# Kernel optimization log

Measured on AMD Instinct MI355X. Metric: run time of the kernel, lower is better.

The kernel has to match this reference:

```python
import jax, jax.numpy as jnp
import numpy as np

B, S, D, H = 4, 1024, 1024, 16
DH = D // H  # head dim = 64
NEG = 1e9  # keras Softmax masking constant for fp32


def setup_inputs() -> dict:
    key = jax.random.key(0)
    ks = jax.random.split(key, 7)
    return {
        "inputs": jax.random.normal(ks[0], (B, S, D), jnp.float32),
        "mask": jax.random.randint(ks[1], (B, 1, 1, S), 0, 2) > 0,
        "interaction": jax.random.normal(ks[2], (B, S, S, H), jnp.float32) * 0.1,
        "W_Q": jax.random.normal(ks[3], (D, D), jnp.float32) * 0.02,
        "W_K": jax.random.normal(ks[4], (D, D), jnp.float32) * 0.02,
        "W_V": jax.random.normal(ks[5], (D, D), jnp.float32) * 0.02,
        "W_O": jax.random.normal(ks[6], (D, D), jnp.float32) * 0.02,
    }


def reference(inputs, mask, interaction, W_Q, W_K, W_V, W_O):
    b, s, d = inputs.shape
    def proj(W):
        # [B,S,D] @ [D,D] -> [B,S,H,DH] -> [B,H,S,DH]
        return (inputs @ W).reshape(b, s, H, DH).transpose(0, 2, 1, 3)
    Q, K, V = proj(W_Q), proj(W_K), proj(W_V)
    scores = jnp.einsum("bhqd,bhkd->bhqk", Q, K) / (DH ** 0.5)
    # interaction [B,S,S,H] -> [B,H,S,S], additive bias before softmax
    scores = scores + interaction.transpose(0, 3, 1, 2)
    # keras Softmax(mask=...): add -1e9 where mask is False, softmax over last axis
    scores = jnp.where(mask, scores, scores - NEG)
    attn = jax.nn.softmax(scores, axis=-1)
    hidden = jnp.einsum("bhqk,bhkd->bhqd", attn, V)
    hidden = hidden.transpose(0, 2, 1, 3).reshape(b, s, d)
    return hidden @ W_O
```

## Files before the change

### kernel.cpp

```cpp
#include <hip/hip_runtime.h>
#include <hip/hip_bf16.h>
#include <stdint.h>

#define BDIM 4
#define SDIM 1024
#define DDIM 1024
#define HDIM 16
#define DHDIM 64

typedef __bf16 bf16_t;
typedef __bf16 bf16x8 __attribute__((ext_vector_type(8)));
typedef __bf16 bf16x4 __attribute__((ext_vector_type(4)));
typedef float f32x4 __attribute__((ext_vector_type(4)));

typedef __attribute__((address_space(3))) uint32_t lds_u32;
typedef const __attribute__((address_space(1))) uint32_t glb_u32;

__device__ __forceinline__ void glds16(const void* g, void* l) {
    __builtin_amdgcn_global_load_lds((glb_u32*)g, (lds_u32*)l, 16, 0, 0);
}


__global__ __launch_bounds__(256) void convert_x_kernel(const float* __restrict__ X,
                                                        bf16_t* __restrict__ Xb, int n) {
    int i = (blockIdx.x * 256 + threadIdx.x) * 4;
    if (i >= n) return;
    float4 v = *(const float4*)(X + i);
    bf16x4 o;
    o[0] = (bf16_t)v.x; o[1] = (bf16_t)v.y; o[2] = (bf16_t)v.z; o[3] = (bf16_t)v.w;
    *(bf16x4*)(Xb + i) = o;
}

__global__ __launch_bounds__(256) void transpose_w_kernel(const float* __restrict__ W0,
                                                          const float* __restrict__ W1,
                                                          const float* __restrict__ W2,
                                                          const float* __restrict__ W3,
                                                          bf16_t* __restrict__ Wt) {
    __shared__ float tile[32][33];
    int z = blockIdx.z;
    const float* W = (z == 0) ? W0 : (z == 1) ? W1 : (z == 2) ? W2 : W3;
    bf16_t* dst = Wt + (size_t)z * DDIM * DDIM;
    int bx = blockIdx.x * 32;
    int by = blockIdx.y * 32;
    int x = threadIdx.x & 31, y0 = threadIdx.x >> 5;
#pragma unroll
    for (int i = 0; i < 4; i++) {
        int y = y0 + i * 8;
        tile[y][x] = W[(size_t)(by + y) * DDIM + bx + x];
    }
    __syncthreads();
#pragma unroll
    for (int i = 0; i < 4; i++) {
        int y = y0 + i * 8;
        dst[(size_t)(bx + y) * DDIM + by + x] = (bf16_t)tile[x][y];
    }
}

__global__ __launch_bounds__(256) void mask_flag_kernel(const unsigned char* __restrict__ mb,
                                                        int* __restrict__ flag) {
    __shared__ int any;
    if (threadIdx.x == 0) any = 0;
    __syncthreads();
    int loc = 0;
    for (int i = threadIdx.x; i < BDIM * SDIM; i += 256)
        if ((i & 3) && mb[i]) loc = 1;
    if (loc) any = 1;
    __syncthreads();
    if (threadIdx.x == 0) *flag = any ? 1 : 0;
}

__global__ __launch_bounds__(256) void bias_tr_kernel(const float* __restrict__ inter,
                                                      const unsigned char* __restrict__ maskb,
                                                      const int* __restrict__ flagp,
                                                      bf16_t* __restrict__ biasT) {
    constexpr int QS = 72;
    constexpr int HS = 16 * 72 + 8;
    __shared__ bf16_t tile[16 * HS];
    __shared__ float pen[64];
    const int k0 = blockIdx.x * 64;
    const int q0 = blockIdx.y * 16;
    const int b  = blockIdx.z;
    const int t = threadIdx.x;
    const int mstride = (*flagp) ? 1 : 4;
    if (t < 64)
        pen[t] = maskb[((size_t)b * SDIM + k0 + t) * mstride] ? 0.f : 1.0e9f;

    const float* src = inter + (((size_t)b * SDIM + q0) * SDIM + k0) * HDIM;
    const int k = t >> 2, h = (t & 3) * 4;
#pragma unroll
    for (int q = 0; q < 16; q++) {
        float4 v = *(const float4*)(src + (size_t)q * SDIM * HDIM + t * 4);
        tile[(h + 0) * HS + q * QS + k] = (bf16_t)v.x;
        tile[(h + 1) * HS + q * QS + k] = (bf16_t)v.y;
        tile[(h + 2) * HS + q * QS + k] = (bf16_t)v.z;
        tile[(h + 3) * HS + q * QS + k] = (bf16_t)v.w;
    }
    __syncthreads();
#pragma unroll
    for (int p = 0; p < 8; p++) {
        int row = p * 32 + (t >> 3);
        int hh = row >> 4, qq = row & 15;
        int kc = (t & 7) * 8;
        bf16x8 vv = *(const bf16x8*)(tile + hh * HS + qq * QS + kc);
        bf16x8 ov;
#pragma unroll
        for (int u = 0; u < 8; u++) ov[u] = (bf16_t)((float)vv[u] - pen[kc + u]);
        *(bf16x8*)(biasT + ((size_t)(b * HDIM + hh) * SDIM + q0 + qq) * SDIM + k0 + kc) = ov;
    }
}

template <int MODE>
__global__ __launch_bounds__(256) void gemm_bt_kernel(const bf16_t* __restrict__ A,
                                                      const bf16_t* __restrict__ Bt,
                                                      bf16_t* __restrict__ Qo, bf16_t* __restrict__ Ko,
                                                      bf16_t* __restrict__ Vo, float* __restrict__ Co) {
    __shared__ bf16_t As[128 * 32];
    __shared__ bf16_t Bs[128 * 32];
    const int m0 = blockIdx.x * 128;
    const int n0 = blockIdx.y * 128;
    const int t = threadIdx.x;
    const int lane = t & 63, w = t >> 6;
    const int wm = w & 1, wn = w >> 1;
    const int low = lane & 15, quad = lane >> 4;
    f32x4 acc[4][4] = {};

    const int srow = w * 16 + (lane >> 2);
    const int koff = (lane & 3) * 8;
    const bf16_t* Ag = A + (size_t)(m0 + srow) * DDIM + koff;
    const bf16_t* Bg = Bt + (size_t)(n0 + srow) * DDIM + koff;
    bf16_t* AsW = As + w * 512;
    bf16_t* BsW = Bs + w * 512;

    for (int k0 = 0; k0 < DDIM; k0 += 32) {
        __syncthreads();
        glds16(Ag + k0, AsW);
        glds16(Ag + (size_t)64 * DDIM + k0, AsW + 64 * 32);
        glds16(Bg + k0, BsW);
        glds16(Bg + (size_t)64 * DDIM + k0, BsW + 64 * 32);
        __syncthreads();
        bf16x8 af[4], bv[4];
#pragma unroll
        for (int mt = 0; mt < 4; mt++)
            af[mt] = *(const bf16x8*)(As + (wm * 64 + mt * 16 + low) * 32 + quad * 8);
#pragma unroll
        for (int nt = 0; nt < 4; nt++)
            bv[nt] = *(const bf16x8*)(Bs + (wn * 64 + nt * 16 + low) * 32 + quad * 8);
#pragma unroll
        for (int mt = 0; mt < 4; mt++)
#pragma unroll
            for (int nt = 0; nt < 4; nt++)
                acc[mt][nt] = __builtin_amdgcn_mfma_f32_16x16x32_bf16(af[mt], bv[nt], acc[mt][nt], 0, 0, 0);
    }

#pragma unroll
    for (int mt = 0; mt < 4; mt++) {
#pragma unroll
        for (int nt = 0; nt < 4; nt++) {
#pragma unroll
            for (int r = 0; r < 4; r++) {
                int mrow = m0 + wm * 64 + mt * 16 + quad * 4 + r;
                int ncol = n0 + wn * 64 + nt * 16 + low;
                float vv = acc[mt][nt][r];
                if (MODE == 0) {
                    int which = ncol >> 10, nl = ncol & 1023;
                    int h = nl >> 6, dh = nl & 63;
                    int b = mrow >> 10, s = mrow & 1023;
                    size_t idx = ((size_t)(b * HDIM + h) * SDIM + s) * DHDIM + dh;
                    if (which == 0) Qo[idx] = (bf16_t)(vv * 0.125f);
                    else if (which == 1) Ko[idx] = (bf16_t)vv;
                    else Vo[idx] = (bf16_t)vv;
                } else {
                    Co[(size_t)mrow * DDIM + ncol] = vv;
                }
            }
        }
    }
}

__global__ __launch_bounds__(256) void attn_kernel(const bf16_t* __restrict__ Q,
                                                   const bf16_t* __restrict__ K,
                                                   const bf16_t* __restrict__ V,
                                                   const bf16_t* __restrict__ biasT,
                                                   bf16_t* __restrict__ hid) {
    __shared__ bf16_t Vt[64 * 72];
    __shared__ bf16_t P[4][16 * 72];
    const int bh = blockIdx.x;
    const int b = bh >> 4, h = bh & 15;
    const int q0 = blockIdx.y * 64;
    const int t = threadIdx.x;
    const int w = t >> 6, lane = t & 63;
    const int low = lane & 15, quad = lane >> 4;

    const bf16_t* Qb = Q + (size_t)bh * SDIM * DHDIM;
    const bf16_t* Kb = K + (size_t)bh * SDIM * DHDIM;
    const bf16_t* Vb = V + (size_t)bh * SDIM * DHDIM;
    const bf16_t* biasB = biasT + (size_t)bh * SDIM * SDIM;

    const int qrow = q0 + w * 16 + low;
    bf16x8 qf0 = *(const bf16x8*)(Qb + (size_t)qrow * DHDIM + quad * 8);
    bf16x8 qf1 = *(const bf16x8*)(Qb + (size_t)qrow * DHDIM + 32 + quad * 8);

    const int qr = q0 + w * 16 + quad * 4;

    float mrow[4], lrow[4];
    f32x4 accO[4] = {};
#pragma unroll
    for (int r = 0; r < 4; r++) { mrow[r] = -3.0e38f; lrow[r] = 0.f; }

    for (int kt = 0; kt < SDIM / 64; kt++) {
        const int kbase = kt * 64;
        __syncthreads();
        {
            int c0 = t, c1 = t + 256;
            int key0 = c0 >> 3, d0 = (c0 & 7) * 8;
            int key1 = c1 >> 3, d1 = (c1 & 7) * 8;
            bf16x8 v0 = *(const bf16x8*)(Vb + (size_t)(kbase + key0) * DHDIM + d0);
            bf16x8 v1 = *(const bf16x8*)(Vb + (size_t)(kbase + key1) * DHDIM + d1);
#pragma unroll
            for (int u = 0; u < 8; u++) Vt[(d0 + u) * 72 + key0] = v0[u];
#pragma unroll
            for (int u = 0; u < 8; u++) Vt[(d1 + u) * 72 + key1] = v1[u];
        }
        f32x4 sacc[4];
#pragma unroll
        for (int nt = 0; nt < 4; nt++) {
            int krow = kbase + nt * 16 + low;
            bf16x8 kf0 = *(const bf16x8*)(Kb + (size_t)krow * DHDIM + quad * 8);
            bf16x8 kf1 = *(const bf16x8*)(Kb + (size_t)krow * DHDIM + 32 + quad * 8);
            f32x4 z = {};
            z = __builtin_amdgcn_mfma_f32_16x16x32_bf16(qf0, kf0, z, 0, 0, 0);
            z = __builtin_amdgcn_mfma_f32_16x16x32_bf16(qf1, kf1, z, 0, 0, 0);
            sacc[nt] = z;
        }
        __syncthreads();
        float sv[4][4];
#pragma unroll
        for (int nt = 0; nt < 4; nt++) {
            int kk = kbase + nt * 16 + low;
#pragma unroll
            for (int r = 0; r < 4; r++) {
                float biasv = (float)biasB[(size_t)(qr + r) * SDIM + kk];
                sv[nt][r] = sacc[nt][r] + biasv;
            }
        }
#pragma unroll
        for (int r = 0; r < 4; r++) {
            float vmx = fmaxf(fmaxf(sv[0][r], sv[1][r]), fmaxf(sv[2][r], sv[3][r]));
            vmx = fmaxf(vmx, __shfl_xor(vmx, 1));
            vmx = fmaxf(vmx, __shfl_xor(vmx, 2));
            vmx = fmaxf(vmx, __shfl_xor(vmx, 4));
            vmx = fmaxf(vmx, __shfl_xor(vmx, 8));
            float mn = fmaxf(mrow[r], vmx);
            float alpha = __expf(mrow[r] - mn);
            mrow[r] = mn;
            lrow[r] *= alpha;
#pragma unroll
            for (int nt = 0; nt < 4; nt++) accO[nt][r] *= alpha;
            float rs = 0.f;
#pragma unroll
            for (int nt = 0; nt < 4; nt++) {
                float p = __expf(sv[nt][r] - mn);
                sv[nt][r] = p;
                rs += p;
            }
            rs += __shfl_xor(rs, 1);
            rs += __shfl_xor(rs, 2);
            rs += __shfl_xor(rs, 4);
            rs += __shfl_xor(rs, 8);
            lrow[r] += rs;
        }
        bf16_t* Pw = &P[w][0];
#pragma unroll
        for (int nt = 0; nt < 4; nt++)
#pragma unroll
            for (int r = 0; r < 4; r++)
                Pw[(quad * 4 + r) * 72 + nt * 16 + low] = (bf16_t)sv[nt][r];
        __syncthreads();
#pragma unroll
        for (int step = 0; step < 2; step++) {
            bf16x8 pf = *(const bf16x8*)(Pw + low * 72 + step * 32 + quad * 8);
#pragma unroll
            for (int nt = 0; nt < 4; nt++) {
                bf16x8 vf = *(const bf16x8*)(Vt + (nt * 16 + low) * 72 + step * 32 + quad * 8);
                accO[nt] = __builtin_amdgcn_mfma_f32_16x16x32_bf16(pf, vf, accO[nt], 0, 0, 0);
            }
        }
    }
#pragma unroll
    for (int r = 0; r < 4; r++) {
        float inv = 1.f / lrow[r];
#pragma unroll
        for (int nt = 0; nt < 4; nt++) {
            hid[((size_t)b * SDIM + (qr + r)) * DDIM + h * 64 + nt * 16 + low] =
                (bf16_t)(accO[nt][r] * inv);
        }
    }
}


extern "C" void kernel_launch(void* const* d_in, const int* in_sizes, int n_in,
                              void* d_out, int out_size, void* d_ws, size_t ws_size,
                              hipStream_t stream) {
    const float* X = (const float*)d_in[0];
    const unsigned char* maskb = (const unsigned char*)d_in[1];
    const float* inter = (const float*)d_in[2];
    const float* WQ = (const float*)d_in[3];
    const float* WK = (const float*)d_in[4];
    const float* WV = (const float*)d_in[5];
    const float* WO = (const float*)d_in[6];
    float* out = (float*)d_out;

    char* ws = (char*)d_ws;
    const size_t MB = 1024 * 1024;
    bf16_t* Xb    = (bf16_t*)(ws + 0 * MB);
    bf16_t* Wt    = (bf16_t*)(ws + 8 * MB);
    bf16_t* Qm    = (bf16_t*)(ws + 16 * MB);
    bf16_t* Km    = (bf16_t*)(ws + 24 * MB);
    bf16_t* Vm    = (bf16_t*)(ws + 32 * MB);
    bf16_t* hid   = (bf16_t*)(ws + 40 * MB);
    int* flag     = (int*)(ws + 48 * MB);
    bf16_t* biasT = (bf16_t*)(ws + 64 * MB);

    convert_x_kernel<<<BDIM * SDIM * DDIM / (256 * 4), 256, 0, stream>>>(X, Xb, BDIM * SDIM * DDIM);
    transpose_w_kernel<<<dim3(32, 32, 4), 256, 0, stream>>>(WQ, WK, WV, WO, Wt);
    mask_flag_kernel<<<1, 256, 0, stream>>>(maskb, flag);
    bias_tr_kernel<<<dim3(16, 64, 4), 256, 0, stream>>>(inter, maskb, flag, biasT);
    gemm_bt_kernel<0><<<dim3(32, 24), 256, 0, stream>>>(Xb, Wt, Qm, Km, Vm, nullptr);
    attn_kernel<<<dim3(BDIM * HDIM, SDIM / 64), 256, 0, stream>>>(Qm, Km, Vm, biasT, hid);
    gemm_bt_kernel<1><<<dim3(32, 8), 256, 0, stream>>>(hid, Wt + (size_t)3 * DDIM * DDIM,
                                                       nullptr, nullptr, nullptr, out);
}
```

Before: 570.0 us.

## Write V pre-transposed from QKV GEMM and drop block syncs in attention

The QKV projection epilogue now writes V in a [dh, s] transposed layout, so the attention kernel reads V^T fragments straight from global memory and no longer builds a transposed V tile in LDS. Each wave works independently with a per-wave fp32 LDS scratch that re-lays scores into row-per-lane form, which removes every __syncthreads and loads bias as contiguous bf16x8 vectors instead of scattered scalars. Softmax bookkeeping changes to one running max per lane with a cross-quad shuffle reduction, and occupancy is hinted via launch_bounds(256,4). The transposed V stores in the GEMM epilogue are strided, K and V are re-read from global by every wave without sharing, and the mask-flag kernel moves to 1024 threads.

```diff
diff --git a/kernel.cpp b/kernel.cpp
--- a/kernel.cpp
+++ b/kernel.cpp
@@ -56,13 +56,13 @@
     }
 }
 
-__global__ __launch_bounds__(256) void mask_flag_kernel(const unsigned char* __restrict__ mb,
-                                                        int* __restrict__ flag) {
+__global__ __launch_bounds__(1024) void mask_flag_kernel(const unsigned char* __restrict__ mb,
+                                                         int* __restrict__ flag) {
     __shared__ int any;
     if (threadIdx.x == 0) any = 0;
     __syncthreads();
     int loc = 0;
-    for (int i = threadIdx.x; i < BDIM * SDIM; i += 256)
+    for (int i = threadIdx.x; i < BDIM * SDIM; i += 1024)
         if ((i & 3) && mb[i]) loc = 1;
     if (loc) any = 1;
     __syncthreads();
@@ -113,7 +113,7 @@
 __global__ __launch_bounds__(256) void gemm_bt_kernel(const bf16_t* __restrict__ A,
                                                       const bf16_t* __restrict__ Bt,
                                                       bf16_t* __restrict__ Qo, bf16_t* __restrict__ Ko,
-                                                      bf16_t* __restrict__ Vo, float* __restrict__ Co) {
+                                                      bf16_t* __restrict__ Vto, float* __restrict__ Co) {
     __shared__ bf16_t As[128 * 32];
     __shared__ bf16_t Bs[128 * 32];
     const int m0 = blockIdx.x * 128;
@@ -165,10 +165,12 @@
                     int which = ncol >> 10, nl = ncol & 1023;
                     int h = nl >> 6, dh = nl & 63;
                     int b = mrow >> 10, s = mrow & 1023;
-                    size_t idx = ((size_t)(b * HDIM + h) * SDIM + s) * DHDIM + dh;
-                    if (which == 0) Qo[idx] = (bf16_t)(vv * 0.125f);
-                    else if (which == 1) Ko[idx] = (bf16_t)vv;
-                    else Vo[idx] = (bf16_t)vv;
+                    if (which == 0)
+                        Qo[((size_t)(b * HDIM + h) * SDIM + s) * DHDIM + dh] = (bf16_t)(vv * 0.125f);
+                    else if (which == 1)
+                        Ko[((size_t)(b * HDIM + h) * SDIM + s) * DHDIM + dh] = (bf16_t)vv;
+                    else
+                        Vto[((size_t)(b * HDIM + h) * DHDIM + dh) * SDIM + s] = (bf16_t)vv;
                 } else {
                     Co[(size_t)mrow * DDIM + ncol] = vv;
                 }
@@ -177,121 +179,113 @@
     }
 }
 
-__global__ __launch_bounds__(256) void attn_kernel(const bf16_t* __restrict__ Q,
-                                                   const bf16_t* __restrict__ K,
-                                                   const bf16_t* __restrict__ V,
-                                                   const bf16_t* __restrict__ biasT,
-                                                   bf16_t* __restrict__ hid) {
-    __shared__ bf16_t Vt[64 * 72];
-    __shared__ bf16_t P[4][16 * 72];
+__global__ __launch_bounds__(256, 4) void attn_kernel(const bf16_t* __restrict__ Q,
+                                                      const bf16_t* __restrict__ K,
+                                                      const bf16_t* __restrict__ Vt,
+                                                      const bf16_t* __restrict__ biasT,
+                                                      bf16_t* __restrict__ hid) {
+    constexpr int KSp = 66;
+    __shared__ float Sl[4][16 * KSp];
     const int bh = blockIdx.x;
     const int b = bh >> 4, h = bh & 15;
-    const int q0 = blockIdx.y * 64;
     const int t = threadIdx.x;
     const int w = t >> 6, lane = t & 63;
     const int low = lane & 15, quad = lane >> 4;
-
-    const bf16_t* Qb = Q + (size_t)bh * SDIM * DHDIM;
+    const int q0 = (blockIdx.y * 4 + w) * 16;
+
+    const bf16_t* Qb = Q + ((size_t)bh * SDIM + q0) * DHDIM;
     const bf16_t* Kb = K + (size_t)bh * SDIM * DHDIM;
-    const bf16_t* Vb = V + (size_t)bh * SDIM * DHDIM;
-    const bf16_t* biasB = biasT + (size_t)bh * SDIM * SDIM;
-
-    const int qrow = q0 + w * 16 + low;
-    bf16x8 qf0 = *(const bf16x8*)(Qb + (size_t)qrow * DHDIM + quad * 8);
-    bf16x8 qf1 = *(const bf16x8*)(Qb + (size_t)qrow * DHDIM + 32 + quad * 8);
-
-    const int qr = q0 + w * 16 + quad * 4;
-
-    float mrow[4], lrow[4];
+    const bf16_t* VtB = Vt + (size_t)bh * DHDIM * SDIM;
+    const bf16_t* biasB = biasT + ((size_t)bh * SDIM + q0 + low) * SDIM;
+    float* Sw = &Sl[w][0];
+
+    bf16x8 qf0 = *(const bf16x8*)(Qb + low * DHDIM + quad * 8);
+    bf16x8 qf1 = *(const bf16x8*)(Qb + low * DHDIM + 32 + quad * 8);
+
+    float mrow = -3.0e38f;
+    float lpart = 0.f;
     f32x4 accO[4] = {};
-#pragma unroll
-    for (int r = 0; r < 4; r++) { mrow[r] = -3.0e38f; lrow[r] = 0.f; }
-
-    for (int kt = 0; kt < SDIM / 64; kt++) {
-        const int kbase = kt * 64;
-        __syncthreads();
-        {
-            int c0 = t, c1 = t + 256;
-            int key0 = c0 >> 3, d0 = (c0 & 7) * 8;
-            int key1 = c1 >> 3, d1 = (c1 & 7) * 8;
-            bf16x8 v0 = *(const bf16x8*)(Vb + (size_t)(kbase + key0) * DHDIM + d0);
-            bf16x8 v1 = *(const bf16x8*)(Vb + (size_t)(kbase + key1) * DHDIM + d1);
-#pragma unroll
-            for (int u = 0; u < 8; u++) Vt[(d0 + u) * 72 + key0] = v0[u];
-#pragma unroll
-            for (int u = 0; u < 8; u++) Vt[(d1 + u) * 72 + key1] = v1[u];
-        }
+
+    for (int c = 0; c < SDIM / 64; c++) {
+        const int kbase = c * 64;
+        bf16x8 bb0 = *(const bf16x8*)(biasB + kbase + quad * 8);
+        bf16x8 bb1 = *(const bf16x8*)(biasB + kbase + 32 + quad * 8);
         f32x4 sacc[4];
 #pragma unroll
         for (int nt = 0; nt < 4; nt++) {
-            int krow = kbase + nt * 16 + low;
-            bf16x8 kf0 = *(const bf16x8*)(Kb + (size_t)krow * DHDIM + quad * 8);
-            bf16x8 kf1 = *(const bf16x8*)(Kb + (size_t)krow * DHDIM + 32 + quad * 8);
+            const bf16_t* kp = Kb + (size_t)(kbase + nt * 16 + low) * DHDIM;
+            bf16x8 kf0 = *(const bf16x8*)(kp + quad * 8);
+            bf16x8 kf1 = *(const bf16x8*)(kp + 32 + quad * 8);
             f32x4 z = {};
             z = __builtin_amdgcn_mfma_f32_16x16x32_bf16(qf0, kf0, z, 0, 0, 0);
             z = __builtin_amdgcn_mfma_f32_16x16x32_bf16(qf1, kf1, z, 0, 0, 0);
             sacc[nt] = z;
         }
-        __syncthreads();
-        float sv[4][4];
+#pragma unroll
+        for (int nt = 0; nt < 4; nt++)
+#pragma unroll
+            for (int r = 0; r < 4; r++)
+                Sw[(quad * 4 + r) * KSp + nt * 16 + low] = sacc[nt][r];
+        float4 a0 = *(const float4*)(Sw + low * KSp + quad * 8);
+        float4 a1 = *(const float4*)(Sw + low * KSp + quad * 8 + 4);
+        float4 a2 = *(const float4*)(Sw + low * KSp + 32 + quad * 8);
+        float4 a3 = *(const float4*)(Sw + low * KSp + 32 + quad * 8 + 4);
+        float sj[16];
+        sj[0] = a0.x + (float)bb0[0]; sj[1] = a0.y + (float)bb0[1];
+        sj[2] = a0.z + (float)bb0[2]; sj[3] = a0.w + (float)bb0[3];
+        sj[4] = a1.x + (float)bb0[4]; sj[5] = a1.y + (float)bb0[5];
+        sj[6] = a1.z + (float)bb0[6]; sj[7] = a1.w + (float)bb0[7];
+        sj[8] = a2.x + (float)bb1[0]; sj[9] = a2.y + (float)bb1[1];
+        sj[10] = a2.z + (float)bb1[2]; sj[11] = a2.w + (float)bb1[3];
+        sj[12] = a3.x + (float)bb1[4]; sj[13] = a3.y + (float)bb1[5];
+        sj[14] = a3.z + (float)bb1[6]; sj[15] = a3.w + (float)bb1[7];
+        float mx = sj[0];
+#pragma unroll
+        for (int j = 1; j < 16; j++) mx = fmaxf(mx, sj[j]);
+        mx = fmaxf(mx, __shfl_xor(mx, 16));
+        mx = fmaxf(mx, __shfl_xor(mx, 32));
+        float mn = fmaxf(mrow, mx);
+        float alpha = __expf(mrow - mn);
+        mrow = mn;
+        lpart *= alpha;
+        float ss = 0.f;
+#pragma unroll
+        for (int j = 0; j < 16; j++) {
+            float p = __expf(sj[j] - mn);
+            sj[j] = p;
+            ss += p;
+        }
+        lpart += ss;
+        float ar[4];
+#pragma unroll
+        for (int r = 0; r < 4; r++) ar[r] = __shfl(alpha, (lane & 48) + quad * 4 + r);
+#pragma unroll
+        for (int nt = 0; nt < 4; nt++)
+#pragma unroll
+            for (int r = 0; r < 4; r++) accO[nt][r] *= ar[r];
+        bf16x8 pf0, pf1;
+#pragma unroll
+        for (int j = 0; j < 8; j++) { pf0[j] = (bf16_t)sj[j]; pf1[j] = (bf16_t)sj[8 + j]; }
 #pragma unroll
         for (int nt = 0; nt < 4; nt++) {
-            int kk = kbase + nt * 16 + low;
-#pragma unroll
-            for (int r = 0; r < 4; r++) {
-                float biasv = (float)biasB[(size_t)(qr + r) * SDIM + kk];
-                sv[nt][r] = sacc[nt][r] + biasv;
-            }
-        }
-#pragma unroll
-        for (int r = 0; r < 4; r++) {
-            float vmx = fmaxf(fmaxf(sv[0][r], sv[1][r]), fmaxf(sv[2][r], sv[3][r]));
-            vmx = fmaxf(vmx, __shfl_xor(vmx, 1));
-            vmx = fmaxf(vmx, __shfl_xor(vmx, 2));
-            vmx = fmaxf(vmx, __shfl_xor(vmx, 4));
-            vmx = fmaxf(vmx, __shfl_xor(vmx, 8));
-            float mn = fmaxf(mrow[r], vmx);
-            float alpha = __expf(mrow[r] - mn);
-            mrow[r] = mn;
-            lrow[r] *= alpha;
-#pragma unroll
-            for (int nt = 0; nt < 4; nt++) accO[nt][r] *= alpha;
-            float rs = 0.f;
-#pragma unroll
-            for (int nt = 0; nt < 4; nt++) {
-                float p = __expf(sv[nt][r] - mn);
-                sv[nt][r] = p;
-                rs += p;
-            }
-            rs += __shfl_xor(rs, 1);
-            rs += __shfl_xor(rs, 2);
-            rs += __shfl_xor(rs, 4);
-            rs += __shfl_xor(rs, 8);
-            lrow[r] += rs;
-        }
-        bf16_t* Pw = &P[w][0];
-#pragma unroll
-        for (int nt = 0; nt < 4; nt++)
-#pragma unroll
-            for (int r = 0; r < 4; r++)
-                Pw[(quad * 4 + r) * 72 + nt * 16 + low] = (bf16_t)sv[nt][r];
-        __syncthreads();
-#pragma unroll
-        for (int step = 0; step < 2; step++) {
-            bf16x8 pf = *(const bf16x8*)(Pw + low * 72 + step * 32 + quad * 8);
-#pragma unroll
-            for (int nt = 0; nt < 4; nt++) {
-                bf16x8 vf = *(const bf16x8*)(Vt + (nt * 16 + low) * 72 + step * 32 + quad * 8);
-                accO[nt] = __builtin_amdgcn_mfma_f32_16x16x32_bf16(pf, vf, accO[nt], 0, 0, 0);
-            }
-        }
-    }
+            const bf16_t* vp = VtB + (size_t)(nt * 16 + low) * SDIM + kbase;
+            bf16x8 vf0 = *(const bf16x8*)(vp + quad * 8);
+            bf16x8 vf1 = *(const bf16x8*)(vp + 32 + quad * 8);
+            accO[nt] = __builtin_amdgcn_mfma_f32_16x16x32_bf16(pf0, vf0, accO[nt], 0, 0, 0);
+            accO[nt] = __builtin_amdgcn_mfma_f32_16x16x32_bf16(pf1, vf1, accO[nt], 0, 0, 0);
+        }
+    }
+    lpart += __shfl_xor(lpart, 16);
+    lpart += __shfl_xor(lpart, 32);
+    float lr[4];
+#pragma unroll
+    for (int r = 0; r < 4; r++) lr[r] = __shfl(lpart, (lane & 48) + quad * 4 + r);
 #pragma unroll
     for (int r = 0; r < 4; r++) {
-        float inv = 1.f / lrow[r];
+        float inv = 1.f / lr[r];
 #pragma unroll
         for (int nt = 0; nt < 4; nt++) {
-            hid[((size_t)b * SDIM + (qr + r)) * DDIM + h * 64 + nt * 16 + low] =
+            hid[((size_t)b * SDIM + q0 + quad * 4 + r) * DDIM + h * 64 + nt * 16 + low] =
                 (bf16_t)(accO[nt][r] * inv);
         }
     }
@@ -316,17 +310,17 @@
     bf16_t* Wt    = (bf16_t*)(ws + 8 * MB);
     bf16_t* Qm    = (bf16_t*)(ws + 16 * MB);
     bf16_t* Km    = (bf16_t*)(ws + 24 * MB);
-    bf16_t* Vm    = (bf16_t*)(ws + 32 * MB);
+    bf16_t* Vtm   = (bf16_t*)(ws + 32 * MB);
     bf16_t* hid   = (bf16_t*)(ws + 40 * MB);
     int* flag     = (int*)(ws + 48 * MB);
     bf16_t* biasT = (bf16_t*)(ws + 64 * MB);
 
     convert_x_kernel<<<BDIM * SDIM * DDIM / (256 * 4), 256, 0, stream>>>(X, Xb, BDIM * SDIM * DDIM);
     transpose_w_kernel<<<dim3(32, 32, 4), 256, 0, stream>>>(WQ, WK, WV, WO, Wt);
-    mask_flag_kernel<<<1, 256, 0, stream>>>(maskb, flag);
+    mask_flag_kernel<<<1, 1024, 0, stream>>>(maskb, flag);
     bias_tr_kernel<<<dim3(16, 64, 4), 256, 0, stream>>>(inter, maskb, flag, biasT);
-    gemm_bt_kernel<0><<<dim3(32, 24), 256, 0, stream>>>(Xb, Wt, Qm, Km, Vm, nullptr);
-    attn_kernel<<<dim3(BDIM * HDIM, SDIM / 64), 256, 0, stream>>>(Qm, Km, Vm, biasT, hid);
+    gemm_bt_kernel<0><<<dim3(32, 24), 256, 0, stream>>>(Xb, Wt, Qm, Km, Vtm, nullptr);
+    attn_kernel<<<dim3(BDIM * HDIM, SDIM / 64), 256, 0, stream>>>(Qm, Km, Vtm, biasT, hid);
     gemm_bt_kernel<1><<<dim3(32, 8), 256, 0, stream>>>(hid, Wt + (size_t)3 * DDIM * DDIM,
                                                        nullptr, nullptr, nullptr, out);
 }
```

Result: slower. 631.3 us (+10.8%).
